# Optimization experiments

Measured on AMD Instinct MI355X. Metric: run time of the kernel, lower is better.

The kernel has to match this reference:

```python
import jax, jax.numpy as jnp
import numpy as np

N_NODES = 10000
N_REL = 40
N_BASES = 30
HIDDEN = 100
N_EDGES = 320000


def setup_inputs() -> dict:
    key = jax.random.key(0)
    ks = jax.random.split(key, 11)
    s = 0.05  # param init scale
    inp = {
        "comp1": jax.random.normal(ks[0], (N_REL, N_BASES), jnp.float32) * s,
        "basis1": jax.random.normal(ks[1], (N_BASES, N_NODES, HIDDEN), jnp.float32) * s,
        "root1": jax.random.normal(ks[2], (N_NODES, HIDDEN), jnp.float32) * s,
        "bias1": jax.random.normal(ks[3], (HIDDEN,), jnp.float32) * s,
        "comp2": jax.random.normal(ks[4], (N_REL, N_BASES), jnp.float32) * s,
        "basis2": jax.random.normal(ks[5], (N_BASES, HIDDEN, HIDDEN), jnp.float32) * s,
        "root2": jax.random.normal(ks[6], (HIDDEN, HIDDEN), jnp.float32) * s,
        "bias2": jax.random.normal(ks[7], (HIDDEN,), jnp.float32) * s,
        "emb_rel": jax.random.normal(ks[8], (N_REL + 1, HIDDEN), jnp.float32) * s,
        "edge_index": jax.random.randint(ks[9], (2, N_EDGES), 0, N_NODES, jnp.int64),
        "edge_type": jax.random.randint(ks[10], (N_EDGES,), 0, N_REL, jnp.int64),
    }
    return inp


def _agg_mean_per_relation(msg, dst, rel, n_nodes, n_rel):
    # PyG RGCNConv loops over relations with aggr='mean': messages are
    # mean-aggregated per (target node, relation), then summed over relations.
    seg = dst * n_rel + rel  # combined (node, relation) segment id
    sums = jax.ops.segment_sum(msg, seg, num_segments=n_nodes * n_rel)
    ones = jnp.ones((msg.shape[0], 1), msg.dtype)
    cnt = jax.ops.segment_sum(ones, seg, num_segments=n_nodes * n_rel)
    mean = sums / jnp.maximum(cnt, 1.0)
    return mean.reshape(n_nodes, n_rel, -1).sum(axis=1)  # [N, hidden]


def reference(comp1, basis1, root1, bias1, comp2, basis2, root2, bias2,
              emb_rel, edge_index, edge_type):
    src, dst = edge_index[0], edge_index[1]
    n_nodes = root1.shape[0]
    n_rel = comp1.shape[0]

    # ---- conv1 (x = None -> featureless: weight acts as embedding over node ids)
    # basis decomposition: W1[r] = sum_b comp1[r,b] * basis1[b]
    W1 = jnp.einsum('rb,bno->rno', comp1, basis1)  # [R, N, H]
    msg1 = W1[edge_type, src]                       # per-edge gather [E, H]
    agg1 = _agg_mean_per_relation(msg1, dst, edge_type, n_nodes, n_rel)
    # root term with x=None is root1[arange(N)] = root1 itself
    h = jax.nn.relu(agg1 + root1 + bias1)           # [N, H]

    # ---- conv2 (dense node features)
    W2 = jnp.einsum('rb,bdo->rdo', comp2, basis2)   # [R, H, H]
    Hx = jnp.einsum('nd,rdo->rno', h, W2)           # all-relation transforms [R, N, H]
    msg2 = Hx[edge_type, src]                       # [E, H]
    agg2 = _agg_mean_per_relation(msg2, dst, edge_type, n_nodes, n_rel)
    x = agg2 + h @ root2 + bias2                    # [N, H]

    # ---- relation embedding lookup (padding_idx=0 -> row 0 is zero)
    emb = emb_rel.at[0].set(0.0)
    rel_embedded = emb[edge_type]                   # [E, H]
    return (x, rel_embedded)
```

## Files before the change

kernel.cpp:

```cpp
#include <hip/hip_runtime.h>
#include <hip/hip_bf16.h>
#include <cstdint>
#include <cstddef>

#define E_EDGES 320000
#define NN 10000
#define NRELS 40
#define NB 30
#define HID 100
#define NHTOT (NN*HID)
#define R2 41
#define KTOT 4224
#define NROWS_PAD 10048
#define SPLITK 4
#define KB_PER 33

typedef short bf16x8 __attribute__((ext_vector_type(8)));
typedef float f32x4 __attribute__((ext_vector_type(4)));
typedef float f32x2 __attribute__((ext_vector_type(2)));

__device__ inline ushort f2bf(float f) {
  uint x = __float_as_uint(f);
  return (ushort)((x + 0x7fffu + ((x >> 16) & 1u)) >> 16);
}
__device__ inline float bflo(uint u) { return __uint_as_float(u << 16); }
__device__ inline float bfhi(uint u) { return __uint_as_float(u & 0xffff0000u); }

__device__ inline uint pack2bf(float x, float y) {
  union { __hip_bfloat162 b; uint u; } cv;
  cv.b = __float22bfloat162_rn(make_float2(x, y));
  return cv.u;
}

__device__ inline void gload16(const void* g, void* l) {
  __builtin_amdgcn_global_load_lds(
      (const __attribute__((address_space(1))) void*)g,
      (__attribute__((address_space(3))) void*)l, 16, 0, 0);
}

__global__ void k_zero(int4* __restrict__ p, int n4) {
  int i = blockIdx.x * 256 + threadIdx.x;
  if (i < n4) p[i] = make_int4(0, 0, 0, 0);
}

__global__ void k_count(const int* __restrict__ dst, const int* __restrict__ et,
                        int* __restrict__ cnt_nr, int* __restrict__ deg) {
  int e = blockIdx.x * blockDim.x + threadIdx.x;
  if (e >= E_EDGES) return;
  int d = dst[e], r = et[e];
  atomicAdd(&cnt_nr[d * NRELS + r], 1);
  atomicAdd(&deg[d], 1);
}

__global__ void k_scan(const int* __restrict__ deg, int* __restrict__ rowptr) {
  __shared__ int ssum[256];
  int t = threadIdx.x;
  const int per = (NN + 255) / 256;
  int base = t * per;
  int s = 0;
  for (int k = 0; k < per; ++k) { int i = base + k; if (i < NN) s += deg[i]; }
  ssum[t] = s; __syncthreads();
  for (int off = 1; off < 256; off <<= 1) {
    int v = (t >= off) ? ssum[t - off] : 0;
    __syncthreads();
    ssum[t] += v;
    __syncthreads();
  }
  int pre = (t == 0) ? 0 : ssum[t - 1];
  for (int k = 0; k < per; ++k) {
    int i = base + k;
    if (i < NN) { rowptr[i] = pre; pre += deg[i]; }
  }
  if (t == 255) rowptr[NN] = ssum[255];
}

__global__ void k_pnr(const int* __restrict__ cnt_nr, const int* __restrict__ rowptr,
                      int2* __restrict__ desc) {
  int n = blockIdx.x * 256 + threadIdx.x;
  if (n >= NN) return;
  int s = rowptr[n];
  for (int r = 0; r < NRELS; ++r) {
    int c = cnt_nr[n * NRELS + r];
    desc[n * NRELS + r] = make_int2(s, c);
    s += c;
  }
}

__global__ void k_bucket(const int* __restrict__ src, const int* __restrict__ dst,
                         const int* __restrict__ et, const int2* __restrict__ desc,
                         int* __restrict__ fill_nr, int* __restrict__ ebuf) {
  int e = blockIdx.x * blockDim.x + threadIdx.x;
  if (e >= E_EDGES) return;
  int d = dst[e], r = et[e];
  int pos = desc[d * NRELS + r].x + atomicAdd(&fill_nr[d * NRELS + r], 1);
  ebuf[pos] = (src[e] << 6) | r;
}

__global__ void k_ct(const float* __restrict__ comp1, float* __restrict__ comp1t) {
  int i = blockIdx.x * 256 + threadIdx.x;
  if (i >= NRELS * NB) return;
  int r = i / NB, b = i - r * NB;
  comp1t[b * NRELS + r] = comp1[i];
}

__global__ __launch_bounds__(256, 2) void k_w1b(const float* __restrict__ comp1t,
                                                const float* __restrict__ basis1,
                                                ushort* __restrict__ W1bs) {
  int i = blockIdx.x * 256 + threadIdx.x;
  if (i >= NHTOT) return;
  float acc[NRELS];
#pragma unroll
  for (int r = 0; r < NRELS; ++r) acc[r] = 0.f;
  for (int b = 0; b < NB; ++b) {
    float v = basis1[(size_t)b * NHTOT + i];
    const float* ct = comp1t + b * NRELS;
#pragma unroll
    for (int r = 0; r < NRELS; ++r) acc[r] += ct[r] * v;
  }
#pragma unroll
  for (int r = 0; r < NRELS; ++r)
    W1bs[(size_t)r * NHTOT + i] = f2bf(acc[r]);
}

__global__ void k_w2(const float* __restrict__ comp2, const float* __restrict__ basis2,
                     float* __restrict__ W2f) {
  int i = blockIdx.x * 256 + threadIdx.x;
  if (i >= HID * HID) return;
  float v[NB];
#pragma unroll
  for (int b = 0; b < NB; ++b) v[b] = basis2[b * HID * HID + i];
  for (int r = 0; r < NRELS; ++r) {
    float a = 0.f;
#pragma unroll
    for (int b = 0; b < NB; ++b) a += comp2[r * NB + b] * v[b];
    W2f[r * HID * HID + i] = a;
  }
}

__global__ void k_bt(const float* __restrict__ W2f, const float* __restrict__ root2,
                     ushort* __restrict__ Bt) {
  int i = blockIdx.x * 256 + threadIdx.x;
  if (i >= 112 * KTOT) return;
  int col = i / KTOT, kk = i - col * KTOT;
  float v = 0.f;
  if (kk < R2 * HID && col < HID) {
    int r = kk / HID, k = kk - r * HID;
    v = (r < NRELS) ? W2f[(r * HID + k) * HID + col] : root2[k * HID + col];
  }
  Bt[i] = f2bf(v);
}

__global__ __launch_bounds__(256) void k_agg1(const int* __restrict__ rowptr,
                                              const int* __restrict__ ebuf,
                                              const int* __restrict__ cnt_nr,
                                              const uint2* __restrict__ W1bf2,
                                              const float4* __restrict__ root1,
                                              const float4* __restrict__ bias1,
                                              float4* __restrict__ h4) {
  __shared__ f32x4 red[10][25];
  int n = blockIdx.x, t = threadIdx.x;
  int g = t / 25, c = t - g * 25;
  if (g < 10) {
    f32x4 a = (f32x4){0.f, 0.f, 0.f, 0.f};
    int beg = rowptr[n], end = rowptr[n + 1];
    for (int j = beg + g; j < end; j += 10) {
      int pk = ebuf[j];
      int r = pk & 63, s = pk >> 6;
      float cf = 1.0f / (float)cnt_nr[n * NRELS + r];
      uint2 u = W1bf2[(size_t)r * 250000 + s * 25 + c];
      a[0] += cf * bflo(u.x); a[1] += cf * bfhi(u.x);
      a[2] += cf * bflo(u.y); a[3] += cf * bfhi(u.y);
    }
    red[g][c] = a;
  }
  __syncthreads();
  if (t < 25) {
    f32x4 a = red[0][t];
#pragma unroll
    for (int g2 = 1; g2 < 10; ++g2) a += red[g2][t];
    float4 rt = root1[n * 25 + t];
    float4 bs = bias1[t];
    a += (f32x4){rt.x, rt.y, rt.z, rt.w};
    a += (f32x4){bs.x, bs.y, bs.z, bs.w};
#pragma unroll
    for (int q = 0; q < 4; ++q) if (a[q] < 0.f) a[q] = 0.f;
    h4[n * 25 + t] = make_float4(a[0], a[1], a[2], a[3]);
  }
}

__global__ __launch_bounds__(512) void k_hseg(const int2* __restrict__ desc,
                                              const int* __restrict__ ebuf,
                                              const f32x4* __restrict__ h4,
                                              uint2* __restrict__ hbar2) {
  int wv = blockIdx.x * 8 + (threadIdx.x >> 6);
  int task = wv * 2 + ((threadIdx.x >> 5) & 1);
  if (task >= NN * R2) return;
  int n = task / R2, r = task - n * R2;
  int lane = threadIdx.x & 31;
  uint2* orow = hbar2 + (size_t)n * (KTOT / 4);
  if (r == NRELS) {
    if (lane < 25) {
      f32x4 v = h4[n * 25 + lane];
      orow[NRELS * 25 + lane] = make_uint2(pack2bf(v[0], v[1]), pack2bf(v[2], v[3]));
    }
    return;
  }
  int2 d = desc[n * NRELS + r];
  if (lane < 25) {
    f32x4 a = (f32x4){0.f, 0.f, 0.f, 0.f};
    for (int j = 0; j < d.y; ++j) {
      int s = ebuf[d.x + j] >> 6;
      a += h4[s * 25 + lane];
    }
    float coef = d.y ? 1.0f / (float)d.y : 0.f;
    a *= coef;
    orow[r * 25 + lane] = make_uint2(pack2bf(a[0], a[1]), pack2bf(a[2], a[3]));
  } else if (r < 28) {
    int idx = r * 7 + (lane - 25);
    if (idx < 31) orow[R2 * 25 + idx] = make_uint2(0u, 0u);
  }
}

__global__ __launch_bounds__(256) void k_gemm(const ushort* __restrict__ hbar,
                                              const ushort* __restrict__ Bt,
                                              float* __restrict__ part) {
  __shared__ char lds[2][12288];
  int t = threadIdx.x;
  int wid = t >> 6, l = t & 63;
  int lrow = l & 15, g16 = l >> 4;
  int kb0 = blockIdx.y * KB_PER;
  int row0 = blockIdx.x * 64;

  f32x4 acc[7];
#pragma unroll
  for (int j = 0; j < 7; ++j) acc[j] = (f32x4){0.f, 0.f, 0.f, 0.f};

  auto stage = [&](int p, int buf) {
    int kbg = kb0 + p;
#pragma unroll
    for (int ci = 0; ci < 3; ++ci) {
      int qb = (wid * 3 + ci) * 64;
      int q = qb + l;
      const ushort* g;
      if (q < 448) {
        int col = q >> 2, c = q & 3;
        g = Bt + (size_t)col * KTOT + kbg * 32 + c * 8;
      } else if (q < 704) {
        int qq = q - 448;
        int row = qq >> 2, c = qq & 3;
        g = hbar + (size_t)(row0 + row) * KTOT + kbg * 32 + c * 8;
      } else {
        g = Bt;
      }
      gload16(g, &lds[buf][(size_t)qb * 16]);
    }
  };

  stage(0, 0);
  __syncthreads();

  int cur = 0;
  for (int p = 0; p < KB_PER; ++p) {
    if (p + 1 < KB_PER) stage(p + 1, cur ^ 1);
    const char* base = lds[cur];
    bf16x8 a = *(const bf16x8*)(base + 7168 + (wid * 16 + lrow) * 64 + g16 * 16);
#pragma unroll
    for (int j = 0; j < 7; ++j) {
      bf16x8 b = *(const bf16x8*)(base + (j * 16 + lrow) * 64 + g16 * 16);
      acc[j] = __builtin_amdgcn_mfma_f32_16x16x32_bf16(a, b, acc[j], 0, 0, 0);
    }
    __syncthreads();
    cur ^= 1;
  }

  float* pp = part + (size_t)blockIdx.y * NROWS_PAD * 112;
  int srow = row0 + wid * 16 + g16 * 4;
#pragma unroll
  for (int j = 0; j < 7; ++j) {
    int col = j * 16 + lrow;
#pragma unroll
    for (int v = 0; v < 4; ++v)
      pp[(size_t)(srow + v) * 112 + col] = acc[j][v];
  }
}

__global__ void k_red(const float* __restrict__ part, const float* __restrict__ bias2,
                      float* __restrict__ xout) {
  int i = blockIdx.x * 256 + threadIdx.x;
  if (i >= NHTOT) return;
  int n = i / HID, c = i - n * HID;
  float s = bias2[c];
#pragma unroll
  for (int g = 0; g < SPLITK; ++g)
    s += part[(size_t)g * NROWS_PAD * 112 + (size_t)n * 112 + c];
  xout[i] = s;
}

__global__ void k_emb(const float4* __restrict__ emb, const int* __restrict__ et,
                      float4* __restrict__ out2) {
  int i = blockIdx.x * 256 + threadIdx.x;
  if (i >= E_EDGES * 25) return;
  int e = i / 25, q = i - e * 25;
  int r = et[e];
  float4 v;
  if (r == 0) { v.x = 0.f; v.y = 0.f; v.z = 0.f; v.w = 0.f; }
  else v = emb[r * 25 + q];
  out2[i] = v;
}

extern "C" void kernel_launch(void* const* d_in, const int* in_sizes, int n_in,
                              void* d_out, int out_size, void* d_ws, size_t ws_size,
                              hipStream_t stream) {
  (void)in_sizes; (void)n_in; (void)out_size; (void)d_ws; (void)ws_size;

  const float* comp1  = (const float*)d_in[0];
  const float* basis1 = (const float*)d_in[1];
  const float* root1  = (const float*)d_in[2];
  const float* bias1  = (const float*)d_in[3];
  const float* comp2  = (const float*)d_in[4];
  const float* basis2 = (const float*)d_in[5];
  const float* root2  = (const float*)d_in[6];
  const float* bias2  = (const float*)d_in[7];
  const float* emb    = (const float*)d_in[8];
  const int*   ei     = (const int*)d_in[9];
  const int*   et     = (const int*)d_in[10];
  const int* srcp = ei;
  const int* dstp = ei + E_EDGES;

  float* xout = (float*)d_out;
  float* scratch = xout + NHTOT;
  int*   cnt_nr = (int*)scratch;
  int*   deg    = cnt_nr + 400000;
  int*   rowptr = deg + 10000;
  int*   fill_nr= rowptr + 10004;
  int2*  desc   = (int2*)(scratch + 820004);
  int*   ebuf   = (int*)(scratch + 1620004);
  float* W2f    = scratch + 1940016;
  ushort* Bt    = (ushort*)(scratch + 2340016);
  float* h      = scratch + 2576560;
  uint*  W1bf   = (uint*)(scratch + 3576560);
  uint*  hbar   = (uint*)(scratch + 3576560);
  float* part   = scratch + 24797936;
  float* comp1t = scratch + 29400000;

  k_zero<<<(205001 + 255) / 256, 256, 0, stream>>>((int4*)cnt_nr, 205001);
  k_zero<<<(25344 + 255) / 256, 256, 0, stream>>>(
      (int4*)((char*)hbar + (size_t)NN * KTOT * 2), 25344);

  k_count <<<(E_EDGES + 255) / 256, 256, 0, stream>>>(dstp, et, cnt_nr, deg);
  k_scan  <<<1, 256, 0, stream>>>(deg, rowptr);
  k_pnr   <<<(NN + 255) / 256, 256, 0, stream>>>(cnt_nr, rowptr, desc);
  k_bucket<<<(E_EDGES + 255) / 256, 256, 0, stream>>>(srcp, dstp, et, desc,
                                                      fill_nr, ebuf);

  k_ct <<<(NRELS * NB + 255) / 256, 256, 0, stream>>>(comp1, comp1t);
  k_w2 <<<(HID * HID + 255) / 256, 256, 0, stream>>>(comp2, basis2, W2f);
  k_bt <<<(112 * KTOT + 255) / 256, 256, 0, stream>>>(W2f, root2, Bt);
  k_w1b<<<(NHTOT + 255) / 256, 256, 0, stream>>>(comp1t, basis1, (ushort*)W1bf);

  k_agg1<<<NN, 256, 0, stream>>>(rowptr, ebuf, cnt_nr, (const uint2*)W1bf,
                                 (const float4*)root1, (const float4*)bias1,
                                 (float4*)h);
  k_hseg<<<(NN * R2 + 15) / 16, 512, 0, stream>>>(desc, ebuf, (const f32x4*)h,
                                                  (uint2*)hbar);
  k_gemm<<<dim3(NROWS_PAD / 64, SPLITK), 256, 0, stream>>>((const ushort*)hbar, Bt, part);
  k_red <<<(NHTOT + 255) / 256, 256, 0, stream>>>(part, bias2, xout);

  k_emb<<<(E_EDGES * 25 + 255) / 256, 256, 0, stream>>>((const float4*)emb, et,
                                                        (float4*)(xout + NHTOT));
}
```

Measured before the change: 281.2 us.

## Compute W1 basis combination with bf16 MFMA and LDS-staged stores

Replaces the scalar FMA kernel that builds W1 = comp1 x basis1 with an MFMA-based kernel. Inputs are converted to bf16, multiplied with 16x16x32 bf16 matrix instructions, and results are staged in shared memory so they can be written out as coalesced 8-byte stores. The goal is to cut ALU cost and register pressure from the 40-accumulator loop. The trade-off is reduced precision, since comp1 and basis1 are now rounded to bf16 before the multiply, and a dependence on the bf16 packing helper.

```diff
diff --git a/kernel.cpp b/kernel.cpp
--- a/kernel.cpp
+++ b/kernel.cpp
@@ -96,30 +96,66 @@
   ebuf[pos] = (src[e] << 6) | r;
 }
 
-__global__ void k_ct(const float* __restrict__ comp1, float* __restrict__ comp1t) {
-  int i = blockIdx.x * 256 + threadIdx.x;
-  if (i >= NRELS * NB) return;
-  int r = i / NB, b = i - r * NB;
-  comp1t[b * NRELS + r] = comp1[i];
-}
-
-__global__ __launch_bounds__(256, 2) void k_w1b(const float* __restrict__ comp1t,
-                                                const float* __restrict__ basis1,
-                                                ushort* __restrict__ W1bs) {
-  int i = blockIdx.x * 256 + threadIdx.x;
-  if (i >= NHTOT) return;
-  float acc[NRELS];
-#pragma unroll
-  for (int r = 0; r < NRELS; ++r) acc[r] = 0.f;
-  for (int b = 0; b < NB; ++b) {
-    float v = basis1[(size_t)b * NHTOT + i];
-    const float* ct = comp1t + b * NRELS;
-#pragma unroll
-    for (int r = 0; r < NRELS; ++r) acc[r] += ct[r] * v;
-  }
-#pragma unroll
-  for (int r = 0; r < NRELS; ++r)
-    W1bs[(size_t)r * NHTOT + i] = f2bf(acc[r]);
+__global__ void k_ct(const float* __restrict__ comp1, ushort* __restrict__ comp1bf) {
+  int i = blockIdx.x * 256 + threadIdx.x;
+  if (i >= 48 * 32) return;
+  int r = i >> 5, b = i & 31;
+  float v = (r < NRELS && b < NB) ? comp1[r * NB + b] : 0.f;
+  comp1bf[i] = f2bf(v);
+}
+
+__global__ __launch_bounds__(256) void k_w1m(const ushort* __restrict__ comp1bf,
+                                             const float* __restrict__ basis1,
+                                             uint2* __restrict__ W1out) {
+  __shared__ ushort st[40][258];
+  int t = threadIdx.x;
+  int w = t >> 6, l = t & 63;
+  int lrow = l & 15, g = l >> 4;
+  int lk = g * 8;
+  size_t i0 = (size_t)blockIdx.x * 256;
+
+  bf16x8 bfr[3];
+#pragma unroll
+  for (int j = 0; j < 3; ++j)
+    bfr[j] = *(const bf16x8*)(comp1bf + (j * 16 + lrow) * 32 + lk);
+
+#pragma unroll
+  for (int rt = 0; rt < 4; ++rt) {
+    size_t ia = i0 + (size_t)w * 64 + rt * 16 + lrow;
+    float f[8];
+#pragma unroll
+    for (int e = 0; e < 8; ++e) {
+      int b = lk + e;
+      f[e] = (b < NB && ia < NHTOT) ? basis1[(size_t)b * NHTOT + ia] : 0.f;
+    }
+    union { uint4 u; bf16x8 v; } au;
+    au.u = make_uint4(pack2bf(f[0], f[1]), pack2bf(f[2], f[3]),
+                      pack2bf(f[4], f[5]), pack2bf(f[6], f[7]));
+    bf16x8 afr = au.v;
+#pragma unroll
+    for (int j = 0; j < 3; ++j) {
+      f32x4 c = __builtin_amdgcn_mfma_f32_16x16x32_bf16(
+          afr, bfr[j], (f32x4){0.f, 0.f, 0.f, 0.f}, 0, 0, 0);
+      int r = j * 16 + lrow;
+      if (r < NRELS) {
+        int iloc = w * 64 + rt * 16 + g * 4;
+        uint* dst = (uint*)&st[r][iloc];
+        dst[0] = pack2bf(c[0], c[1]);
+        dst[1] = pack2bf(c[2], c[3]);
+      }
+    }
+  }
+  __syncthreads();
+  for (int idx = t; idx < NRELS * 64; idx += 256) {
+    int r = idx >> 6, q = idx & 63;
+    size_t gi = i0 + q * 4;
+    if (gi < NHTOT) {
+      const ushort* s = &st[r][q * 4];
+      W1out[((size_t)r * NHTOT + gi) >> 2] =
+          make_uint2((uint)s[0] | ((uint)s[1] << 16),
+                     (uint)s[2] | ((uint)s[3] << 16));
+    }
+  }
 }
 
 __global__ void k_w2(const float* __restrict__ comp2, const float* __restrict__ basis2,
@@ -341,7 +377,7 @@
   uint*  W1bf   = (uint*)(scratch + 3576560);
   uint*  hbar   = (uint*)(scratch + 3576560);
   float* part   = scratch + 24797936;
-  float* comp1t = scratch + 29400000;
+  ushort* comp1bf = (ushort*)(scratch + 29400000);
 
   k_zero<<<(205001 + 255) / 256, 256, 0, stream>>>((int4*)cnt_nr, 205001);
   k_zero<<<(25344 + 255) / 256, 256, 0, stream>>>(
@@ -353,10 +389,10 @@
   k_bucket<<<(E_EDGES + 255) / 256, 256, 0, stream>>>(srcp, dstp, et, desc,
                                                       fill_nr, ebuf);
 
-  k_ct <<<(NRELS * NB + 255) / 256, 256, 0, stream>>>(comp1, comp1t);
+  k_ct <<<(48 * 32 + 255) / 256, 256, 0, stream>>>(comp1, comp1bf);
   k_w2 <<<(HID * HID + 255) / 256, 256, 0, stream>>>(comp2, basis2, W2f);
   k_bt <<<(112 * KTOT + 255) / 256, 256, 0, stream>>>(W2f, root2, Bt);
-  k_w1b<<<(NHTOT + 255) / 256, 256, 0, stream>>>(comp1t, basis1, (ushort*)W1bf);
+  k_w1m<<<(NHTOT + 255) / 256, 256, 0, stream>>>(comp1bf, basis1, (uint2*)W1bf);
 
   k_agg1<<<NN, 256, 0, stream>>>(rowptr, ebuf, cnt_nr, (const uint2*)W1bf,
                                  (const float4*)root1, (const float4*)bias1,
```

Result: no change. 277.4 us (-1.4%).
